# Performance work log

Measured on AMD Instinct MI355X. Metric: run time of the kernel, lower is better.

Reference implementation:

```python
import jax, jax.numpy as jnp
import numpy as np
from jax import lax

DIM = 192
HEADS = 8
HIDDEN = int(DIM * 2.66)  # 510
EPS_LN = 1e-5
EPS_NORM = 1e-12


def conv1x1(x, w):
    # x: (B,C,H,W), w: (O,I,1,1)
    return lax.conv_general_dilated(x, w, (1, 1), 'VALID',
                                    dimension_numbers=('NCHW', 'OIHW', 'NCHW'))


def dwconv3x3(x, w):
    # depthwise 3x3, padding=1; w: (C,1,3,3)
    c = x.shape[1]
    return lax.conv_general_dilated(x, w, (1, 1), 'SAME',
                                    dimension_numbers=('NCHW', 'OIHW', 'NCHW'),
                                    feature_group_count=c)


def layernorm_chan(x, weight, bias):
    # WithBias LayerNorm over channel dim of NCHW (matches to_3d -> LN(-1) -> to_4d)
    mu = jnp.mean(x, axis=1, keepdims=True)
    var = jnp.var(x, axis=1, keepdims=True)
    xn = (x - mu) * lax.rsqrt(var + EPS_LN)
    return xn * weight[None, :, None, None] + bias[None, :, None, None]


def l2norm(x):
    # F.normalize along last dim with eps=1e-12
    n = jnp.sqrt(jnp.sum(x * x, axis=-1, keepdims=True))
    return x / jnp.maximum(n, EPS_NORM)


def attention(x, temperature, w_qkv, w_qkv_dw, w_proj):
    b, c, h, w = x.shape
    hw = h * w
    head_dim = c // HEADS
    qkv = dwconv3x3(conv1x1(x, w_qkv), w_qkv_dw)  # (B, 3C, H, W)
    q, k, v = jnp.split(qkv, 3, axis=1)
    q = l2norm(q.reshape(b, HEADS, head_dim, hw))
    k = l2norm(k.reshape(b, HEADS, head_dim, hw))
    v = v.reshape(b, HEADS, head_dim, hw)
    # channel-wise attention: (B,H,d,d)
    attn = jnp.einsum('bhde,bhce->bhdc', q, k) * temperature[None]
    attn = jax.nn.softmax(attn, axis=-1)
    out = jnp.einsum('bhdc,bhce->bhde', attn, v).reshape(b, c, h, w)
    return conv1x1(out, w_proj)


def ffn(x, w_in, w_dw, w_out):
    x = conv1x1(x, w_in)                 # (B, 2*hidden, H, W)
    x = dwconv3x3(x, w_dw)
    x1, x2 = jnp.split(x, 2, axis=1)
    x = jax.nn.gelu(x1, approximate=False) * x2
    return conv1x1(x, w_out)


def setup_inputs() -> dict:
    key = jax.random.key(0)
    ks = jax.random.split(key, 8)
    b, c, h, w = 4, DIM, 128, 128
    s = 0.05
    return {
        'x': jax.random.normal(ks[0], (b, c, h, w), jnp.float32),
        'temperature': jnp.ones((HEADS, 1, 1), jnp.float32),
        'ln1_w': jnp.ones((c,), jnp.float32),
        'ln1_b': jnp.zeros((c,), jnp.float32),
        'ln2_w': jnp.ones((c,), jnp.float32),
        'ln2_b': jnp.zeros((c,), jnp.float32),
        'w_qkv': jax.random.normal(ks[1], (3 * c, c, 1, 1), jnp.float32) * s,
        'w_qkv_dw': jax.random.normal(ks[2], (3 * c, 1, 3, 3), jnp.float32) * s,
        'w_proj': jax.random.normal(ks[3], (c, c, 1, 1), jnp.float32) * s,
        'w_in': jax.random.normal(ks[4], (2 * HIDDEN, c, 1, 1), jnp.float32) * s,
        'w_dw': jax.random.normal(ks[5], (2 * HIDDEN, 1, 3, 3), jnp.float32) * s,
        'w_out_ffn': jax.random.normal(ks[6], (c, HIDDEN, 1, 1), jnp.float32) * s,
    }


def reference(x, temperature, ln1_w, ln1_b, ln2_w, ln2_b, w_qkv, w_qkv_dw,
              w_proj, w_in, w_dw, w_out_ffn):
    x = x + attention(layernorm_chan(x, ln1_w, ln1_b), temperature,
                      w_qkv, w_qkv_dw, w_proj)
    x = x + ffn(layernorm_chan(x, ln2_w, ln2_b), w_in, w_dw, w_out_ffn)
    return x
```

## Files before the change

kernel.cpp:

```cpp
#include <hip/hip_runtime.h>
#include <hip/hip_bf16.h>
#include <math.h>


#define HW_ 16384

typedef __attribute__((ext_vector_type(8))) short bf16x8;
typedef __attribute__((ext_vector_type(4))) float f32x4;
typedef __attribute__((ext_vector_type(16))) float f32x16;
typedef __attribute__((ext_vector_type(4))) int i32x4;

union Pack8 { __hip_bfloat16 h[8]; i32x4 v; };

__global__ __launch_bounds__(256) void convert_weights(
    const float* __restrict__ wqkv, const float* __restrict__ wproj,
    const float* __restrict__ win, const float* __restrict__ wout,
    __hip_bfloat16* __restrict__ oq, __hip_bfloat16* __restrict__ op,
    __hip_bfloat16* __restrict__ oi, __hip_bfloat16* __restrict__ oo) {
  const int i = blockIdx.x * 256 + threadIdx.x;
  if (i < 110592) oq[i] = __float2bfloat16(wqkv[i]);
  if (i < 36864)  op[i] = __float2bfloat16(wproj[i]);
  if (i < 196608) {
    int m = i / 192, k = i - m * 192;
    oi[i] = __float2bfloat16(m < 1020 ? win[m * 192 + k] : 0.f);
  }
  if (i < 98304) {
    int m = i >> 9, k = i & 511;
    oo[i] = __float2bfloat16(k < 510 ? wout[m * 510 + k] : 0.f);
  }
}

__global__ __launch_bounds__(256) void ln_t_kernel(
    const float* __restrict__ x, const float* __restrict__ w,
    const float* __restrict__ bi, __hip_bfloat16* __restrict__ yt) {
  const int b = blockIdx.y;
  x += (size_t)b * 192 * HW_;
  yt += (size_t)b * HW_ * 192;
  __shared__ float tile[192][68];
  __shared__ float psum[4][64], psq[4][64];
  __shared__ float mu_s[64], inv_s[64];
  const int tid = threadIdx.x;
  const int p0 = blockIdx.x * 64;
  for (int idx = tid; idx < 192 * 16; idx += 256) {
    int c = idx >> 4, p4 = idx & 15;
    f32x4 v = *(const f32x4*)(x + (size_t)c * HW_ + p0 + p4 * 4);
    *(f32x4*)&tile[c][p4 * 4] = v;
  }
  __syncthreads();
  const int tx = tid & 63, ty = tid >> 6;
  float s = 0.f, s2 = 0.f;
  for (int c = ty * 48; c < ty * 48 + 48; c++) {
    float v = tile[c][tx]; s += v; s2 += v * v;
  }
  psum[ty][tx] = s; psq[ty][tx] = s2;
  __syncthreads();
  if (ty == 0) {
    float ts = psum[0][tx] + psum[1][tx] + psum[2][tx] + psum[3][tx];
    float ts2 = psq[0][tx] + psq[1][tx] + psq[2][tx] + psq[3][tx];
    float mu = ts * (1.f / 192.f);
    float var = ts2 * (1.f / 192.f) - mu * mu;
    mu_s[tx] = mu; inv_s[tx] = rsqrtf(var + 1e-5f);
  }
  __syncthreads();
  for (int idx = tid; idx < 64 * 24; idx += 256) {
    int c8 = idx % 24, p = idx / 24;
    float mu = mu_s[p], inv = inv_s[p];
    Pack8 pk;
    #pragma unroll
    for (int u = 0; u < 8; u++) {
      int c = c8 * 8 + u;
      pk.h[u] = __float2bfloat16((tile[c][p] - mu) * inv * w[c] + bi[c]);
    }
    *(i32x4*)&yt[(size_t)(p0 + p) * 192 + c8 * 8] = pk.v;
  }
}

__global__ __launch_bounds__(256) void gemm_bstat(
    const __hip_bfloat16* __restrict__ A, const __hip_bfloat16* __restrict__ Bg,
    __hip_bfloat16* __restrict__ Dout, int Mtiles, size_t Bstr, size_t Dstr) {
  const int z = blockIdx.y;
  const __hip_bfloat16* B = Bg + (size_t)z * Bstr;
  __hip_bfloat16* D = Dout + (size_t)z * Dstr;
  const int col0 = blockIdx.x * 128;
  __shared__ __align__(16) __hip_bfloat16 Bs[128][192];
  __shared__ __align__(16) __hip_bfloat16 As[64][192];
  const int tid = threadIdx.x;
  const int wave = tid >> 6, lane = tid & 63;
  const int quad = lane >> 4, lr = lane & 15;
  const int wm = (wave & 1) * 32, wn = (wave >> 1) * 64;
  const int lrx = lr & 7;

  const int arow = tid >> 3, ach = tid & 7;
  const int achs = ach ^ (arow & 7);

  #pragma unroll
  for (int l = 0; l < 4; l++) {
    const int row = arow + 32 * l;
    const __hip_bfloat16* bp = B + (size_t)(col0 + row) * 192;
    #pragma unroll
    for (int j = 0; j < 3; j++) {
      i32x4 v = *(const i32x4*)(bp + (ach + 8 * j) * 8);
      *(i32x4*)&Bs[row][(achs + 8 * j) * 8] = v;
    }
  }
  i32x4 areg[6];
  #pragma unroll
  for (int l = 0; l < 2; l++)
    #pragma unroll
    for (int j = 0; j < 3; j++)
      areg[l * 3 + j] = *(const i32x4*)(
          A + (size_t)(arow + 32 * l) * 192 + (ach + 8 * j) * 8);
  #pragma unroll
  for (int l = 0; l < 2; l++)
    #pragma unroll
    for (int j = 0; j < 3; j++)
      *(i32x4*)&As[arow + 32 * l][(achs + 8 * j) * 8] = areg[l * 3 + j];
  __syncthreads();

  for (int mt = 0; mt < Mtiles; mt++) {
    const int row0 = mt * 64;
    if (mt + 1 < Mtiles) {
      const __hip_bfloat16* ap = A + (size_t)(mt + 1) * 64 * 192;
      #pragma unroll
      for (int l = 0; l < 2; l++)
        #pragma unroll
        for (int j = 0; j < 3; j++)
          areg[l * 3 + j] = *(const i32x4*)(
              ap + (size_t)(arow + 32 * l) * 192 + (ach + 8 * j) * 8);
    }
    f32x4 acc[2][4];
    #pragma unroll
    for (int i = 0; i < 2; i++)
      #pragma unroll
      for (int j = 0; j < 4; j++) acc[i][j] = (f32x4){0.f, 0.f, 0.f, 0.f};
    #pragma unroll
    for (int kc = 0; kc < 6; kc++) {
      const int chq = ((kc * 4 + quad) ^ lrx) * 8;
      bf16x8 a0 = *(const bf16x8*)&As[wm + lr][chq];
      bf16x8 a1 = *(const bf16x8*)&As[wm + 16 + lr][chq];
      #pragma unroll
      for (int j = 0; j < 4; j++) {
        bf16x8 bb = *(const bf16x8*)&Bs[wn + j * 16 + lr][chq];
        acc[0][j] = __builtin_amdgcn_mfma_f32_16x16x32_bf16(a0, bb, acc[0][j], 0, 0, 0);
        acc[1][j] = __builtin_amdgcn_mfma_f32_16x16x32_bf16(a1, bb, acc[1][j], 0, 0, 0);
      }
    }
    #pragma unroll
    for (int i = 0; i < 2; i++)
      #pragma unroll
      for (int r = 0; r < 4; r++) {
        const int gm = row0 + wm + i * 16 + quad * 4 + r;
        __hip_bfloat16* dp = D + (size_t)gm * HW_ + col0 + wn + lr;
        #pragma unroll
        for (int j = 0; j < 4; j++)
          dp[j * 16] = __float2bfloat16(acc[i][j][r]);
      }
    __syncthreads();
    if (mt + 1 < Mtiles) {
      #pragma unroll
      for (int l = 0; l < 2; l++)
        #pragma unroll
        for (int j = 0; j < 3; j++)
          *(i32x4*)&As[arow + 32 * l][(achs + 8 * j) * 8] = areg[l * 3 + j];
      __syncthreads();
    }
  }
}

template <int EPI>
__global__ __launch_bounds__(256) void mfma_gemm(
    const __hip_bfloat16* __restrict__ A, const __hip_bfloat16* __restrict__ Bg,
    const float* __restrict__ Cres, void* __restrict__ Dout,
    int M, int N, int K, size_t Bstr, size_t Cstr, size_t Dstr) {
  const int z = blockIdx.z;
  const __hip_bfloat16* B = Bg + (size_t)z * Bstr;
  const float* C = Cres ? Cres + (size_t)z * Cstr : nullptr;
  __shared__ __align__(16) __hip_bfloat16 As[64][64];
  __shared__ __align__(16) __hip_bfloat16 Bs[128][64];
  const int tid = threadIdx.x;
  const int wave = tid >> 6, lane = tid & 63;
  const int quad = lane >> 4, lr = lane & 15;
  const int lrx = lr & 7;
  const int wm = (wave & 1) * 32, wn = (wave >> 1) * 64;
  const int row0 = blockIdx.x * 64, col0 = blockIdx.y * 128;

  f32x4 acc[2][4];
  #pragma unroll
  for (int i = 0; i < 2; i++)
    #pragma unroll
    for (int j = 0; j < 4; j++) acc[i][j] = (f32x4){0.f, 0.f, 0.f, 0.f};

  for (int k0 = 0; k0 < K; k0 += 64) {
    #pragma unroll
    for (int l = 0; l < 2; l++) {
      int t = tid + l * 256;
      int row = t >> 3, ch = t & 7;
      i32x4 v = *(const i32x4*)(A + (size_t)(row0 + row) * K + k0 + ch * 8);
      *(i32x4*)&As[row][(ch ^ (row & 7)) * 8] = v;
    }
    #pragma unroll
    for (int l = 0; l < 4; l++) {
      int t = tid + l * 256;
      int row = t >> 3, ch = t & 7;
      i32x4 v = *(const i32x4*)(B + (size_t)(col0 + row) * K + k0 + ch * 8);
      *(i32x4*)&Bs[row][(ch ^ (row & 7)) * 8] = v;
    }
    __syncthreads();
    #pragma unroll
    for (int ks = 0; ks < 2; ks++) {
      const int chq = ((ks * 4 + quad) ^ lrx) * 8;
      bf16x8 a0 = *(const bf16x8*)&As[wm + lr][chq];
      bf16x8 a1 = *(const bf16x8*)&As[wm + 16 + lr][chq];
      #pragma unroll
      for (int j = 0; j < 4; j++) {
        bf16x8 bb = *(const bf16x8*)&Bs[wn + j * 16 + lr][chq];
        acc[0][j] = __builtin_amdgcn_mfma_f32_16x16x32_bf16(a0, bb, acc[0][j], 0, 0, 0);
        acc[1][j] = __builtin_amdgcn_mfma_f32_16x16x32_bf16(a1, bb, acc[1][j], 0, 0, 0);
      }
    }
    __syncthreads();
  }

  #pragma unroll
  for (int i = 0; i < 2; i++) {
    #pragma unroll
    for (int r = 0; r < 4; r++) {
      int gm = row0 + wm + i * 16 + quad * 4 + r;
      if (gm >= M) continue;
      #pragma unroll
      for (int j = 0; j < 4; j++) {
        int gn = col0 + wn + j * 16 + lr;
        size_t idx = (size_t)gm * N + gn;
        if (EPI == 0) {
          (((__hip_bfloat16*)Dout) + (size_t)z * Dstr)[idx] = __float2bfloat16(acc[i][j][r]);
        } else {
          (((float*)Dout) + (size_t)z * Dstr)[idx] = acc[i][j][r] + C[idx];
        }
      }
    }
  }
}

__global__ __launch_bounds__(256) void dw_kernel(
    const __hip_bfloat16* __restrict__ in, const float* __restrict__ wdw,
    __hip_bfloat16* __restrict__ out, float* __restrict__ nrm2p) {
  const int b = blockIdx.z;
  in  += (size_t)b * 576 * HW_;
  out += (size_t)b * 576 * HW_;
  const int c = blockIdx.y;
  const int x8 = threadIdx.x & 15;
  const int y = blockIdx.x * 16 + (threadIdx.x >> 4);
  const __hip_bfloat16* ip = in + (size_t)c * HW_;
  const float* wp = wdw + c * 9;
  float wv[9];
  #pragma unroll
  for (int u = 0; u < 9; u++) wv[u] = wp[u];
  float acc[8];
  #pragma unroll
  for (int j = 0; j < 8; j++) acc[j] = 0.f;
  #pragma unroll
  for (int r = 0; r < 3; r++) {
    int yy = y + r - 1;
    if (yy < 0 || yy >= 128) continue;
    const __hip_bfloat16* rp = ip + yy * 128 + x8 * 8;
    Pack8 mid; mid.v = *(const i32x4*)rp;
    float row[10];
    row[0] = (x8 > 0) ? (float)rp[-1] : 0.f;
    #pragma unroll
    for (int u = 0; u < 8; u++) row[1 + u] = (float)mid.h[u];
    row[9] = (x8 < 15) ? (float)rp[8] : 0.f;
    const float wl = wv[r * 3], wc = wv[r * 3 + 1], wr = wv[r * 3 + 2];
    #pragma unroll
    for (int j = 0; j < 8; j++)
      acc[j] += wl * row[j] + wc * row[j + 1] + wr * row[j + 2];
  }
  Pack8 o;
  #pragma unroll
  for (int j = 0; j < 8; j++) o.h[j] = __float2bfloat16(acc[j]);
  *(i32x4*)(out + (size_t)c * HW_ + y * 128 + x8 * 8) = o.v;
  if (c < 384) {
    float s = 0.f;
    #pragma unroll
    for (int j = 0; j < 8; j++) s += acc[j] * acc[j];
    #pragma unroll
    for (int off = 32; off > 0; off >>= 1) s += __shfl_down(s, off, 64);
    __shared__ float wsum[4];
    const int lane = threadIdx.x & 63, wvi = threadIdx.x >> 6;
    if (lane == 0) wsum[wvi] = s;
    __syncthreads();
    if (threadIdx.x == 0)
      nrm2p[((size_t)b * 384 + c) * 8 + blockIdx.x] =
          wsum[0] + wsum[1] + wsum[2] + wsum[3];
  }
}

__global__ __launch_bounds__(256) void gram_kernel(
    const __hip_bfloat16* __restrict__ qkv, float* __restrict__ Gpart) {
  const int b = blockIdx.z;
  qkv   += (size_t)b * 576 * HW_;
  Gpart += (size_t)b * 32 * 8 * 576;
  const int h = blockIdx.x, chunk = blockIdx.y;
  const int tid = threadIdx.x;
  const int w = tid >> 6, lane = tid & 63;
  const int m = lane & 31;
  const int khalf = lane >> 5;
  const __hip_bfloat16* qb = qkv + (size_t)(h * 24) * HW_;
  const __hip_bfloat16* kb = qkv + (size_t)(192 + h * 24) * HW_;
  f32x16 acc;
  #pragma unroll
  for (int i = 0; i < 16; i++) acc[i] = 0.f;
  const int e0 = chunk * 512 + w * 128;
  #pragma unroll
  for (int j = 0; j < 8; j++) {
    const int k0 = e0 + j * 16 + khalf * 8;
    bf16x8 a = *(const bf16x8*)(qb + (size_t)m * HW_ + k0);
    bf16x8 bfr = *(const bf16x8*)(kb + (size_t)m * HW_ + k0);
    acc = __builtin_amdgcn_mfma_f32_32x32x16_bf16(a, bfr, acc, 0, 0, 0);
  }
  __shared__ float gs[4][576];
  #pragma unroll
  for (int r = 0; r < 16; r++) {
    int row = (r & 3) + 8 * (r >> 2) + 4 * khalf;
    if (row < 24 && m < 24) gs[w][row * 24 + m] = acc[r];
  }
  __syncthreads();
  float* gp = Gpart + (size_t)(chunk * 8 + h) * 576;
  for (int t = tid; t < 576; t += 256)
    gp[t] = gs[0][t] + gs[1][t] + gs[2][t] + gs[3][t];
}

__global__ __launch_bounds__(256) void softmax2_kernel(
    const float* __restrict__ Gpart, const float* __restrict__ nrm2p,
    const float* __restrict__ temp, float* __restrict__ P) {
  const int b = blockIdx.y;
  Gpart += (size_t)b * 32 * 8 * 576;
  nrm2p += (size_t)b * 384 * 8;
  P     += (size_t)b * 8 * 576;
  const int h = blockIdx.x;
  const int tid = threadIdx.x;
  __shared__ float Gs[576];
  __shared__ float nq[24], nk[24];
  for (int t = tid; t < 576; t += 256) {
    float s = 0.f;
    for (int ch = 0; ch < 32; ch++)
      s += Gpart[(size_t)(ch * 8 + h) * 576 + t];
    Gs[t] = s;
  }
  if (tid < 48) {
    const int r = (tid < 24) ? (h * 24 + tid) : (192 + h * 24 + tid - 24);
    float s = 0.f;
    #pragma unroll
    for (int j = 0; j < 8; j++) s += nrm2p[(size_t)r * 8 + j];
    float nv = fmaxf(sqrtf(s), 1e-12f);
    if (tid < 24) nq[tid] = nv; else nk[tid - 24] = nv;
  }
  __syncthreads();
  if (tid < 24) {
    const int d = tid;
    const float tp = temp[h];
    float row[24], mx = -1e30f;
    #pragma unroll
    for (int c = 0; c < 24; c++) {
      float v = Gs[d * 24 + c] * tp / (nq[d] * nk[c]);
      row[c] = v; mx = fmaxf(mx, v);
    }
    float s = 0.f;
    #pragma unroll
    for (int c = 0; c < 24; c++) { float e = expf(row[c] - mx); row[c] = e; s += e; }
    const float inv = 1.f / s;
    #pragma unroll
    for (int c = 0; c < 24; c++) P[h * 576 + d * 24 + c] = row[c] * inv;
  }
}

__global__ __launch_bounds__(256) void pv_kernel(
    const float* __restrict__ P, const __hip_bfloat16* __restrict__ qkv,
    __hip_bfloat16* __restrict__ yt) {
  const int b = blockIdx.z;
  P   += (size_t)b * 8 * 576;
  qkv += (size_t)b * 576 * HW_;
  yt  += (size_t)b * HW_ * 192;
  const int hh = blockIdx.x;
  const int e = blockIdx.y * 256 + threadIdx.x;
  __shared__ float Ps[576];
  for (int t = threadIdx.x; t < 576; t += 256) Ps[t] = P[hh * 576 + t];
  __syncthreads();
  const __hip_bfloat16* vb = qkv + (size_t)(384 + hh * 24) * HW_;
  float acc[24];
  #pragma unroll
  for (int d = 0; d < 24; d++) acc[d] = 0.f;
  for (int c = 0; c < 24; c++) {
    float v = (float)vb[(size_t)c * HW_ + e];
    #pragma unroll
    for (int d = 0; d < 24; d++) acc[d] += Ps[d * 24 + c] * v;
  }
  #pragma unroll
  for (int g = 0; g < 3; g++) {
    Pack8 pk;
    #pragma unroll
    for (int u = 0; u < 8; u++) pk.h[u] = __float2bfloat16(acc[g * 8 + u]);
    *(i32x4*)&yt[(size_t)e * 192 + hh * 24 + g * 8] = pk.v;
  }
}

__global__ __launch_bounds__(256) void dwg_t_kernel(
    const __hip_bfloat16* __restrict__ hsrc, const float* __restrict__ wdw,
    __hip_bfloat16* __restrict__ gt, int b0) {
  const int z = blockIdx.z;
  const int bb = b0 + z;
  const int yt = blockIdx.x >> 1, xh = blockIdx.x & 1;
  const int cz = blockIdx.y;
  const int tid = threadIdx.x;
  const int cl = tid >> 3, x8 = tid & 7;
  const int c = cz * 32 + cl;
  const int y0 = yt * 8;
  const int pxb = xh * 64 + x8 * 8;
  __shared__ __hip_bfloat16 sg[32][522];

  const bool active = (c < 510);
  const int ca = active ? c : 0;
  const __hip_bfloat16* ha = hsrc + ((size_t)bb * 1024 + ca) * HW_;
  const __hip_bfloat16* hb = hsrc + ((size_t)bb * 1024 + ca + 510) * HW_;
  float wva[9], wvb[9];
  #pragma unroll
  for (int u = 0; u < 9; u++) {
    wva[u] = active ? wdw[c * 9 + u] : 0.f;
    wvb[u] = active ? wdw[(c + 510) * 9 + u] : 0.f;
  }

  float aA[3][8], aB[3][8];
  #pragma unroll
  for (int s = 0; s < 3; s++)
    #pragma unroll
    for (int j = 0; j < 8; j++) { aA[s][j] = 0.f; aB[s][j] = 0.f; }

  #pragma unroll
  for (int i = 0; i < 10; i++) {
    const int ry = y0 - 1 + i;
    float ra[10], rb[10];
    if (ry >= 0 && ry < 128) {
      const int off = ry * 128 + pxb;
      Pack8 ma; ma.v = *(const i32x4*)(ha + off);
      Pack8 mb; mb.v = *(const i32x4*)(hb + off);
      ra[0] = (pxb > 0) ? (float)ha[off - 1] : 0.f;
      rb[0] = (pxb > 0) ? (float)hb[off - 1] : 0.f;
      #pragma unroll
      for (int u = 0; u < 8; u++) { ra[1 + u] = (float)ma.h[u]; rb[1 + u] = (float)mb.h[u]; }
      ra[9] = (pxb < 120) ? (float)ha[off + 8] : 0.f;
      rb[9] = (pxb < 120) ? (float)hb[off + 8] : 0.f;
    } else {
      #pragma unroll
      for (int u = 0; u < 10; u++) { ra[u] = 0.f; rb[u] = 0.f; }
    }
    #pragma unroll
    for (int r = 0; r < 3; r++) {
      const int lo = i - r;
      if (lo < 0 || lo >= 8) continue;
      const int s = lo % 3;
      const float a0 = wva[r * 3], a1 = wva[r * 3 + 1], a2 = wva[r * 3 + 2];
      const float b0w = wvb[r * 3], b1 = wvb[r * 3 + 1], b2 = wvb[r * 3 + 2];
      #pragma unroll
      for (int j = 0; j < 8; j++) {
        aA[s][j] += a0 * ra[j] + a1 * ra[j + 1] + a2 * ra[j + 2];
        aB[s][j] += b0w * rb[j] + b1 * rb[j + 1] + b2 * rb[j + 2];
      }
    }
    {
      const int lo = i - 2;
      if (lo >= 0 && lo < 8) {
        const int s = lo % 3;
        Pack8 o;
        #pragma unroll
        for (int j = 0; j < 8; j++) {
          float v = aA[s][j];
          float ge = 0.5f * v * (1.f + erff(v * 0.70710678118654752f));
          o.h[j] = __float2bfloat16(ge * aB[s][j]);
          aA[s][j] = 0.f; aB[s][j] = 0.f;
        }
        *(i32x4*)&sg[cl][lo * 64 + x8 * 8] = o.v;
      }
    }
  }
  __syncthreads();
  const int sp = tid >> 2, ch0 = (tid & 3) * 8;
  #pragma unroll
  for (int k = 0; k < 8; k++) {
    Pack8 o;
    #pragma unroll
    for (int u = 0; u < 8; u++) o.h[u] = sg[ch0 + u][k * 64 + sp];
    const int gp = (y0 + k) * 128 + xh * 64 + sp;
    *(i32x4*)&gt[((size_t)z * HW_ + gp) * 512 + cz * 32 + ch0] = o.v;
  }
}

extern "C" void kernel_launch(void* const* d_in, const int* in_sizes, int n_in,
                              void* d_out, int out_size, void* d_ws, size_t ws_size,
                              hipStream_t stream) {
  const float* x     = (const float*)d_in[0];
  const float* temp  = (const float*)d_in[1];
  const float* ln1w  = (const float*)d_in[2];
  const float* ln1b  = (const float*)d_in[3];
  const float* ln2w  = (const float*)d_in[4];
  const float* ln2b  = (const float*)d_in[5];
  const float* wqkv  = (const float*)d_in[6];
  const float* wqkvdw= (const float*)d_in[7];
  const float* wproj = (const float*)d_in[8];
  const float* win   = (const float*)d_in[9];
  const float* wdw   = (const float*)d_in[10];
  const float* wout  = (const float*)d_in[11];
  float* out = (float*)d_out;
  char* ws = (char*)d_ws;

  const int HW = 16384;
  const size_t HWC = (size_t)192 * HW;

  __hip_bfloat16* yt    = (__hip_bfloat16*)(ws + 0);
  __hip_bfloat16* qkva  = (__hip_bfloat16*)(ws + 25165824);
  __hip_bfloat16* qkvb  = (__hip_bfloat16*)(ws + 100663296);
  __hip_bfloat16* hbuf  = (__hip_bfloat16*)(ws + 25165824);
  float*          xa    = (float*)(ws + 176160768);
  __hip_bfloat16* gt    = (__hip_bfloat16*)(ws + 226492416);
  __hip_bfloat16* wqkvB = (__hip_bfloat16*)(ws + 260046848);
  __hip_bfloat16* wprojB= (__hip_bfloat16*)(ws + 260268032);
  __hip_bfloat16* winB  = (__hip_bfloat16*)(ws + 260341760);
  __hip_bfloat16* woutB = (__hip_bfloat16*)(ws + 260734976);
  float*          nrm2p = (float*)(ws + 260931584);
  float*          Gpart = (float*)(ws + 260980736);
  float*          P     = (float*)(ws + 263340032);

  convert_weights<<<768, 256, 0, stream>>>(wqkv, wproj, win, wout,
                                           wqkvB, wprojB, winB, woutB);

  ln_t_kernel<<<dim3(256, 4), 256, 0, stream>>>(x, ln1w, ln1b, yt);
  gemm_bstat<<<dim3(128, 4), 256, 0, stream>>>(
      wqkvB, yt, qkva, 9, (size_t)HW * 192, (size_t)576 * HW);
  dw_kernel<<<dim3(8, 576, 4), 256, 0, stream>>>(qkva, wqkvdw, qkvb, nrm2p);
  gram_kernel<<<dim3(8, 32, 4), 256, 0, stream>>>(qkvb, Gpart);
  softmax2_kernel<<<dim3(8, 4), 256, 0, stream>>>(Gpart, nrm2p, temp, P);
  pv_kernel<<<dim3(8, 64, 4), 256, 0, stream>>>(P, qkvb, yt);
  mfma_gemm<1><<<dim3(3, 128, 4), 256, 0, stream>>>(
      wprojB, yt, x, xa, 192, HW, 192,
      (size_t)HW * 192, HWC, HWC);
  ln_t_kernel<<<dim3(256, 4), 256, 0, stream>>>(xa, ln2w, ln2b, yt);
  gemm_bstat<<<dim3(128, 4), 256, 0, stream>>>(
      winB, yt, hbuf, 16, (size_t)HW * 192, (size_t)1024 * HW);
  for (int half = 0; half < 2; half++) {
    const int b0 = half * 2;
    dwg_t_kernel<<<dim3(32, 16, 2), 256, 0, stream>>>(hbuf, wdw, gt, b0);
    mfma_gemm<1><<<dim3(3, 128, 2), 256, 0, stream>>>(
        woutB, gt, xa + (size_t)b0 * HWC, out + (size_t)b0 * HWC,
        192, HW, 512, (size_t)HW * 512, HWC, HWC);
  }
}
```

Before: 486.6 us.

## Load GEMM A-operand directly from global, reuse bstat GEMM for proj, shuffle dwconv halos

The stationary-B GEMM no longer stages the weight (A) tile in shared memory. Each wave reads its A fragments straight from global/L2 into registers, which removes two barriers per M-tile and halves LDS use. The kernel gains a residual-add fp32 epilogue so the output projection can use it in place of the generic tiled GEMM. The depthwise conv now gets its left and right halo elements via wave shuffles instead of extra scalar global loads. The cost is more global A traffic per block and less explicit prefetch overlap.

```diff
diff --git a/kernel.cpp b/kernel.cpp
--- a/kernel.cpp
+++ b/kernel.cpp
@@ -75,15 +75,15 @@
   }
 }
 
+template <int EPI>
 __global__ __launch_bounds__(256) void gemm_bstat(
     const __hip_bfloat16* __restrict__ A, const __hip_bfloat16* __restrict__ Bg,
-    __hip_bfloat16* __restrict__ Dout, int Mtiles, size_t Bstr, size_t Dstr) {
+    const float* __restrict__ Cres, void* __restrict__ Dout,
+    int Mtiles, size_t Bstr, size_t Cstr, size_t Dstr) {
   const int z = blockIdx.y;
   const __hip_bfloat16* B = Bg + (size_t)z * Bstr;
-  __hip_bfloat16* D = Dout + (size_t)z * Dstr;
   const int col0 = blockIdx.x * 128;
   __shared__ __align__(16) __hip_bfloat16 Bs[128][192];
-  __shared__ __align__(16) __hip_bfloat16 As[64][192];
   const int tid = threadIdx.x;
   const int wave = tid >> 6, lane = tid & 63;
   const int quad = lane >> 4, lr = lane & 15;
@@ -92,7 +92,6 @@
 
   const int arow = tid >> 3, ach = tid & 7;
   const int achs = ach ^ (arow & 7);
-
   #pragma unroll
   for (int l = 0; l < 4; l++) {
     const int row = arow + 32 * l;
@@ -103,30 +102,18 @@
       *(i32x4*)&Bs[row][(achs + 8 * j) * 8] = v;
     }
   }
-  i32x4 areg[6];
-  #pragma unroll
-  for (int l = 0; l < 2; l++)
-    #pragma unroll
-    for (int j = 0; j < 3; j++)
-      areg[l * 3 + j] = *(const i32x4*)(
-          A + (size_t)(arow + 32 * l) * 192 + (ach + 8 * j) * 8);
-  #pragma unroll
-  for (int l = 0; l < 2; l++)
-    #pragma unroll
-    for (int j = 0; j < 3; j++)
-      *(i32x4*)&As[arow + 32 * l][(achs + 8 * j) * 8] = areg[l * 3 + j];
-  __syncthreads();
+  __syncthreads();
+
+  const __hip_bfloat16* Ar0 = A + (size_t)(wm + lr) * 192 + quad * 8;
+  const __hip_bfloat16* Ar1 = A + (size_t)(wm + 16 + lr) * 192 + quad * 8;
 
   for (int mt = 0; mt < Mtiles; mt++) {
-    const int row0 = mt * 64;
-    if (mt + 1 < Mtiles) {
-      const __hip_bfloat16* ap = A + (size_t)(mt + 1) * 64 * 192;
-      #pragma unroll
-      for (int l = 0; l < 2; l++)
-        #pragma unroll
-        for (int j = 0; j < 3; j++)
-          areg[l * 3 + j] = *(const i32x4*)(
-              ap + (size_t)(arow + 32 * l) * 192 + (ach + 8 * j) * 8);
+    const size_t abase = (size_t)mt * (64 * 192);
+    bf16x8 a0[6], a1[6];
+    #pragma unroll
+    for (int kc = 0; kc < 6; kc++) {
+      a0[kc] = *(const bf16x8*)(Ar0 + abase + kc * 32);
+      a1[kc] = *(const bf16x8*)(Ar1 + abase + kc * 32);
     }
     f32x4 acc[2][4];
     #pragma unroll
@@ -136,33 +123,31 @@
     #pragma unroll
     for (int kc = 0; kc < 6; kc++) {
       const int chq = ((kc * 4 + quad) ^ lrx) * 8;
-      bf16x8 a0 = *(const bf16x8*)&As[wm + lr][chq];
-      bf16x8 a1 = *(const bf16x8*)&As[wm + 16 + lr][chq];
       #pragma unroll
       for (int j = 0; j < 4; j++) {
         bf16x8 bb = *(const bf16x8*)&Bs[wn + j * 16 + lr][chq];
-        acc[0][j] = __builtin_amdgcn_mfma_f32_16x16x32_bf16(a0, bb, acc[0][j], 0, 0, 0);
-        acc[1][j] = __builtin_amdgcn_mfma_f32_16x16x32_bf16(a1, bb, acc[1][j], 0, 0, 0);
+        acc[0][j] = __builtin_amdgcn_mfma_f32_16x16x32_bf16(a0[kc], bb, acc[0][j], 0, 0, 0);
+        acc[1][j] = __builtin_amdgcn_mfma_f32_16x16x32_bf16(a1[kc], bb, acc[1][j], 0, 0, 0);
       }
     }
-    #pragma unroll
-    for (int i = 0; i < 2; i++)
+    const int row0 = mt * 64;
+    #pragma unroll
+    for (int i = 0; i < 2; i++) {
       #pragma unroll
       for (int r = 0; r < 4; r++) {
         const int gm = row0 + wm + i * 16 + quad * 4 + r;
-        __hip_bfloat16* dp = D + (size_t)gm * HW_ + col0 + wn + lr;
-        #pragma unroll
-        for (int j = 0; j < 4; j++)
-          dp[j * 16] = __float2bfloat16(acc[i][j][r]);
+        const size_t base = (size_t)gm * HW_ + col0 + wn + lr;
+        if (EPI == 0) {
+          __hip_bfloat16* dp = (__hip_bfloat16*)Dout + (size_t)z * Dstr + base;
+          #pragma unroll
+          for (int j = 0; j < 4; j++) dp[j * 16] = __float2bfloat16(acc[i][j][r]);
+        } else {
+          float* dp = (float*)Dout + (size_t)z * Dstr + base;
+          const float* cp = Cres + (size_t)z * Cstr + base;
+          #pragma unroll
+          for (int j = 0; j < 4; j++) dp[j * 16] = acc[i][j][r] + cp[j * 16];
+        }
       }
-    __syncthreads();
-    if (mt + 1 < Mtiles) {
-      #pragma unroll
-      for (int l = 0; l < 2; l++)
-        #pragma unroll
-        for (int j = 0; j < 3; j++)
-          *(i32x4*)&As[arow + 32 * l][(achs + 8 * j) * 8] = areg[l * 3 + j];
-      __syncthreads();
     }
   }
 }
@@ -260,15 +245,20 @@
   for (int j = 0; j < 8; j++) acc[j] = 0.f;
   #pragma unroll
   for (int r = 0; r < 3; r++) {
-    int yy = y + r - 1;
-    if (yy < 0 || yy >= 128) continue;
-    const __hip_bfloat16* rp = ip + yy * 128 + x8 * 8;
-    Pack8 mid; mid.v = *(const i32x4*)rp;
+    const int yy = y + r - 1;
+    const bool valid = (yy >= 0) && (yy < 128);
+    Pack8 mid;
+    if (valid) mid.v = *(const i32x4*)(ip + yy * 128 + x8 * 8);
+    else       mid.v = (i32x4){0, 0, 0, 0};
+    const int hi = ((i32x4)mid.v)[3];
+    const int lo = ((i32x4)mid.v)[0];
+    const int lw = __shfl_up(hi, 1, 64);
+    const int rw = __shfl_down(lo, 1, 64);
     float row[10];
-    row[0] = (x8 > 0) ? (float)rp[-1] : 0.f;
+    row[0] = (x8 > 0) ? (float)(((const __hip_bfloat16*)&lw)[1]) : 0.f;
     #pragma unroll
     for (int u = 0; u < 8; u++) row[1 + u] = (float)mid.h[u];
-    row[9] = (x8 < 15) ? (float)rp[8] : 0.f;
+    row[9] = (x8 < 15) ? (float)(((const __hip_bfloat16*)&rw)[0]) : 0.f;
     const float wl = wv[r * 3], wc = wv[r * 3 + 1], wr = wv[r * 3 + 2];
     #pragma unroll
     for (int j = 0; j < 8; j++)
@@ -532,18 +522,17 @@
                                            wqkvB, wprojB, winB, woutB);
 
   ln_t_kernel<<<dim3(256, 4), 256, 0, stream>>>(x, ln1w, ln1b, yt);
-  gemm_bstat<<<dim3(128, 4), 256, 0, stream>>>(
-      wqkvB, yt, qkva, 9, (size_t)HW * 192, (size_t)576 * HW);
+  gemm_bstat<0><<<dim3(128, 4), 256, 0, stream>>>(
+      wqkvB, yt, nullptr, qkva, 9, (size_t)HW * 192, 0, (size_t)576 * HW);
   dw_kernel<<<dim3(8, 576, 4), 256, 0, stream>>>(qkva, wqkvdw, qkvb, nrm2p);
   gram_kernel<<<dim3(8, 32, 4), 256, 0, stream>>>(qkvb, Gpart);
   softmax2_kernel<<<dim3(8, 4), 256, 0, stream>>>(Gpart, nrm2p, temp, P);
   pv_kernel<<<dim3(8, 64, 4), 256, 0, stream>>>(P, qkvb, yt);
-  mfma_gemm<1><<<dim3(3, 128, 4), 256, 0, stream>>>(
-      wprojB, yt, x, xa, 192, HW, 192,
-      (size_t)HW * 192, HWC, HWC);
+  gemm_bstat<1><<<dim3(128, 4), 256, 0, stream>>>(
+      wprojB, yt, x, xa, 3, (size_t)HW * 192, HWC, HWC);
   ln_t_kernel<<<dim3(256, 4), 256, 0, stream>>>(xa, ln2w, ln2b, yt);
-  gemm_bstat<<<dim3(128, 4), 256, 0, stream>>>(
-      winB, yt, hbuf, 16, (size_t)HW * 192, (size_t)1024 * HW);
+  gemm_bstat<0><<<dim3(128, 4), 256, 0, stream>>>(
+      winB, yt, nullptr, hbuf, 16, (size_t)HW * 192, 0, (size_t)1024 * HW);
   for (int half = 0; half < 2; half++) {
     const int b0 = half * 2;
     dwg_t_kernel<<<dim3(32, 16, 2), 256, 0, stream>>>(hbuf, wdw, gt, b0);
```

Measured after the change: 517.0 us. 6.3% more time.
